# Kernel tuning notes

Hardware: AMD Instinct MI355X
Metric: run time of the kernel (lower is better)

The kernel has to match this reference:

```python
import jax, jax.numpy as jnp
import numpy as np

B, C, H, W = 2, 256, 64, 64
HEADS, DIM_HEAD = 8, 64
INNER = HEADS * DIM_HEAD


def setup_inputs() -> dict:
    key = jax.random.key(0)
    k1, k2, k3, k4 = jax.random.split(key, 4)
    x = jax.random.normal(k1, (B, C, H, W), dtype=jnp.float32)
    # 1x1 conv weights stored as [out_ch, in_ch]
    w_qkv = jax.random.normal(k2, (3 * INNER, C), dtype=jnp.float32) * (1.0 / np.sqrt(C))
    w_out = jax.random.normal(k3, (C, INNER), dtype=jnp.float32) * (1.0 / np.sqrt(INNER))
    b_out = jax.random.normal(k4, (C,), dtype=jnp.float32) * 0.01
    return {"x": x, "w_qkv": w_qkv, "w_out": w_out, "b_out": b_out}


def reference(x, w_qkv, w_out, b_out):
    b, c, h, w = x.shape
    n = h * w
    # 1x1 conv == channel matmul
    qkv = jnp.einsum('oc,bchw->bohw', w_qkv, x)  # [B, 3*inner, H, W]
    qkv = qkv.reshape(b, 3, HEADS, DIM_HEAD, n)
    qkv = jnp.transpose(qkv, (1, 0, 2, 4, 3))    # [3, B, heads, N, dim_head]
    q, k, v = qkv[0], qkv[1], qkv[2]
    scale = 1.0 / (DIM_HEAD ** 0.5)
    dots = jnp.einsum('bhnd,bhmd->bhnm', q, k) * scale  # [B, heads, N, N]
    attn = jax.nn.softmax(dots, axis=-1)
    out = jnp.einsum('bhnm,bhmd->bhnd', attn, v)        # [B, heads, N, dim_head]
    out = jnp.transpose(out, (0, 1, 3, 2)).reshape(b, INNER, h, w)
    return jnp.einsum('ci,bihw->bchw', w_out, out) + b_out[None, :, None, None]
```

## Files before the change

kernel.cpp:

```cpp
#include <hip/hip_runtime.h>
#include <hip/hip_bf16.h>

typedef unsigned short u16;
typedef __attribute__((ext_vector_type(8))) short bf16x8;
typedef __attribute__((ext_vector_type(4))) float f32x4;
typedef __attribute__((ext_vector_type(8))) unsigned short u16x8;
typedef __attribute__((ext_vector_type(4))) unsigned short u16x4;

#define N_POS 4096
#define HEADS 8
#define DHEAD 64
#define CIN   256
#define INNER 512
#define NSPLIT 2
#define JCHUNK (N_POS / NSPLIT)

__device__ __forceinline__ u16 f2bf(float f) {
    union { float f; unsigned int u; } v; v.f = f;
    unsigned int u = v.u + 0x7FFFu + ((v.u >> 16) & 1u);
    return (u16)(u >> 16);
}

__device__ __forceinline__ float bf2f(u16 h) {
    union { float f; unsigned int u; } v; v.u = ((unsigned int)h) << 16;
    return v.f;
}

__device__ __forceinline__ unsigned int pkbf2(float lo, float hi) {
    union { __hip_bfloat162 b; unsigned int u; } cv;
    cv.b = __float22bfloat162_rn(make_float2(lo, hi));
    return cv.u;
}

__global__ __launch_bounds__(256) void k0_prep(const float* __restrict__ x,
                                               const float* __restrict__ w_qkv,
                                               const float* __restrict__ w_out,
                                               u16* __restrict__ xT,
                                               u16* __restrict__ wq,
                                               u16* __restrict__ wo) {
    int bid = blockIdx.x;
    int t   = threadIdx.x;
    if (bid < 256) {
        int b = bid >> 7, rest = bid & 127;
        int n  = (rest & 15) * 256 + t;
        int c0 = (rest >> 4) * 32;
        const float* xp = x + (size_t)b * CIN * N_POS + n;
        u16* op = xT + ((size_t)(b * N_POS + n)) * CIN + c0;
        for (int g = 0; g < 4; ++g) {
            u16x8 v;
            for (int j = 0; j < 8; ++j)
                v[j] = f2bf(xp[(size_t)(c0 + g * 8 + j) * N_POS]);
            *(u16x8*)(op + g * 8) = v;
        }
    } else if (bid < 448) {
        size_t idx = (size_t)(bid - 256) * 2048 + t * 8;
        u16x8 v;
        for (int j = 0; j < 8; ++j) v[j] = f2bf(w_qkv[idx + j]);
        *(u16x8*)(wq + idx) = v;
    } else {
        size_t idx = (size_t)(bid - 448) * 2048 + t * 8;
        u16x8 v;
        for (int j = 0; j < 8; ++j) v[j] = f2bf(w_out[idx + j]);
        *(u16x8*)(wo + idx) = v;
    }
}

__global__ __launch_bounds__(256, 4) void k1_qkv(const u16* __restrict__ wq,
                                                 const u16* __restrict__ xT,
                                                 u16* __restrict__ q_ws,
                                                 u16* __restrict__ k_ws,
                                                 u16* __restrict__ vt_ws) {
    __shared__ u16 Alds[64 * 40];
    __shared__ u16 Blds[128 * 40];
    int tid = threadIdx.x;
    int n0  = blockIdx.x * 128;
    int by  = blockIdx.y;
    int b   = blockIdx.z;
    int o0  = by * 64;
    int sel = by >> 3;
    int h   = by & 7;
    int wv = tid >> 6, l = tid & 63, quad = l >> 4, l15 = l & 15;
    int srow = tid >> 2, sseg = tid & 3;
    int brow = tid >> 1, bseg = tid & 1;

    f32x4 acc[8] = {};
    for (int c0 = 0; c0 < CIN; c0 += 32) {
        *(u16x8*)&Alds[srow * 40 + sseg * 8] =
            *(const u16x8*)(wq + (size_t)(o0 + srow) * CIN + c0 + sseg * 8);
        const u16* xp = xT + ((size_t)(b * N_POS + n0 + brow)) * CIN + c0 + bseg * 16;
        *(u16x8*)&Blds[brow * 40 + bseg * 16]     = *(const u16x8*)xp;
        *(u16x8*)&Blds[brow * 40 + bseg * 16 + 8] = *(const u16x8*)(xp + 8);
        __syncthreads();
        bf16x8 af = *(const bf16x8*)&Alds[(wv * 16 + l15) * 40 + quad * 8];
        if (sel < 2) {
            for (int nt = 0; nt < 8; ++nt) {
                bf16x8 bfrag = *(const bf16x8*)&Blds[(nt * 16 + l15) * 40 + quad * 8];
                acc[nt] = __builtin_amdgcn_mfma_f32_16x16x32_bf16(af, bfrag, acc[nt], 0, 0, 0);
            }
        } else {
            for (int nt = 0; nt < 8; ++nt) {
                bf16x8 bfrag = *(const bf16x8*)&Blds[(nt * 16 + l15) * 40 + quad * 8];
                acc[nt] = __builtin_amdgcn_mfma_f32_16x16x32_bf16(bfrag, af, acc[nt], 0, 0, 0);
            }
        }
        __syncthreads();
    }
    const float QSCALE = 0.125f * 1.44269504088896f;
    int bh = b * HEADS + h;
    if (sel < 2) {
        float sc = (sel == 0) ? QSCALE : 1.0f;
        u16* base = (sel == 0) ? q_ws : k_ws;
        int dbase = wv * 16 + quad * 4;
        for (int nt = 0; nt < 8; ++nt) {
            int n = n0 + nt * 16 + l15;
            u16x4 pk;
            for (int r = 0; r < 4; ++r) pk[r] = f2bf(acc[nt][r] * sc);
            *(u16x4*)&base[((size_t)bh * N_POS + n) * DHEAD + dbase] = pk;
        }
    } else {
        int dloc = wv * 16 + l15;
        for (int nt = 0; nt < 8; ++nt) {
            u16x4 pk;
            for (int r = 0; r < 4; ++r) pk[r] = f2bf(acc[nt][r]);
            *(u16x4*)&vt_ws[((size_t)bh * DHEAD + dloc) * N_POS
                            + n0 + nt * 16 + quad * 4] = pk;
        }
    }
}

__global__ __launch_bounds__(256, 2) void k2_attn(const u16* __restrict__ q_ws,
                                                  const u16* __restrict__ k_ws,
                                                  const u16* __restrict__ vt_ws,
                                                  u16* __restrict__ op_ws,
                                                  float* __restrict__ lw_ws) {
    __shared__ u16 Klds[64 * 72];
    __shared__ u16 Vlds[64 * 72];
    int tid = threadIdx.x;
    int v   = blockIdx.x + (blockIdx.y << 4) + (blockIdx.z << 8);
    int slot = v & 7, idx = v >> 3;
    int bh   = slot * 2 + (idx & 1);
    int q0   = ((idx >> 1) & 15) * 256;
    int half = idx >> 5;
    int jbase = half * JCHUNK;
    int wv = tid >> 6, l = tid & 63, quad = l >> 4, l15 = l & 15;
    int srow = tid >> 2, sseg = tid & 3;
    int srowp = (srow & 0x23) | ((srow & 4) << 2) | ((srow & 0x18) >> 1);

    const u16* qp = q_ws + ((size_t)(bh * N_POS + q0 + wv * 64 + l15)) * DHEAD + quad * 8;
    bf16x8 bq[4][2];
    for (int it = 0; it < 4; ++it) {
        bq[it][0] = *(const bf16x8*)(qp + (size_t)it * 16 * DHEAD);
        bq[it][1] = *(const bf16x8*)(qp + (size_t)it * 16 * DHEAD + 32);
    }

    f32x4 Oacc[4][4] = {};
    float lsum[4] = {0.f, 0.f, 0.f, 0.f};

    const u16* kp = k_ws + ((size_t)(bh * N_POS + srow)) * DHEAD + sseg * 16;
    const u16* vp = vt_ws + ((size_t)(bh * DHEAD + srow)) * N_POS + sseg * 16;

    u16x8 pf0 = *(const u16x8*)(kp + (size_t)jbase * DHEAD);
    u16x8 pf1 = *(const u16x8*)(kp + (size_t)jbase * DHEAD + 8);
    u16x8 pf2 = *(const u16x8*)(vp + jbase);
    u16x8 pf3 = *(const u16x8*)(vp + jbase + 8);

    for (int j0 = jbase; j0 < jbase + JCHUNK; j0 += 64) {
        *(u16x8*)&Klds[srowp * 72 + sseg * 16]     = pf0;
        *(u16x8*)&Klds[srowp * 72 + sseg * 16 + 8] = pf1;
        *(u16x8*)&Vlds[srow * 72 + sseg * 16]      = pf2;
        *(u16x8*)&Vlds[srow * 72 + sseg * 16 + 8]  = pf3;
        __syncthreads();

        if (j0 + 64 < jbase + JCHUNK) {
            const u16* kpj = kp + (size_t)(j0 + 64) * DHEAD;
            pf0 = *(const u16x8*)kpj;
            pf1 = *(const u16x8*)(kpj + 8);
            pf2 = *(const u16x8*)(vp + j0 + 64);
            pf3 = *(const u16x8*)(vp + j0 + 72);
        }

        union PF { unsigned int u[4]; bf16x8 v; };
        PF pfr[4][2];
        for (int p = 0; p < 2; ++p)
            for (int a = 0; a < 2; ++a) {
                const u16* kb = &Klds[((2 * p + a) * 16 + l15) * 72 + quad * 8];
                bf16x8 kf0 = *(const bf16x8*)kb;
                bf16x8 kf1 = *(const bf16x8*)(kb + 32);
                f32x4 z[4];
                __builtin_amdgcn_s_setprio(1);
                for (int it = 0; it < 4; ++it) {
                    f32x4 t = {};
                    t = __builtin_amdgcn_mfma_f32_16x16x32_bf16(kf0, bq[it][0], t, 0, 0, 0);
                    t = __builtin_amdgcn_mfma_f32_16x16x32_bf16(kf1, bq[it][1], t, 0, 0, 0);
                    z[it] = t;
                }
                __builtin_amdgcn_s_setprio(0);
                for (int it = 0; it < 4; ++it) {
                    float e0 = __builtin_amdgcn_exp2f(z[it][0]);
                    float e1 = __builtin_amdgcn_exp2f(z[it][1]);
                    float e2 = __builtin_amdgcn_exp2f(z[it][2]);
                    float e3 = __builtin_amdgcn_exp2f(z[it][3]);
                    lsum[it] += (e0 + e1) + (e2 + e3);
                    pfr[it][p].u[2 * a]     = pkbf2(e0, e1);
                    pfr[it][p].u[2 * a + 1] = pkbf2(e2, e3);
                }
            }

        __builtin_amdgcn_s_setprio(1);
        for (int dt = 0; dt < 4; ++dt)
            for (int p = 0; p < 2; ++p) {
                bf16x8 vf = *(const bf16x8*)&Vlds[(dt * 16 + l15) * 72 + p * 32 + quad * 8];
                for (int it = 0; it < 4; ++it)
                    Oacc[it][dt] = __builtin_amdgcn_mfma_f32_16x16x32_bf16(vf, pfr[it][p].v, Oacc[it][dt], 0, 0, 0);
            }
        __builtin_amdgcn_s_setprio(0);
        __syncthreads();
    }

    int b = bh >> 3, h = bh & 7;
    u16* opb = op_ws + (size_t)half * 2 * N_POS * INNER;
    float* lwb = lw_ws + (size_t)half * 2 * HEADS * N_POS;
    for (int it = 0; it < 4; ++it) {
        float ls = lsum[it];
        ls += __shfl_xor(ls, 16);
        ls += __shfl_xor(ls, 32);
        int n = q0 + wv * 64 + it * 16 + l15;
        if (quad == 0) lwb[(size_t)bh * N_POS + n] = ls;
        u16* dst = opb + ((size_t)(b * N_POS + n)) * INNER + h * DHEAD;
        for (int dt = 0; dt < 4; ++dt) {
            u16x4 pk;
            for (int r = 0; r < 4; ++r) pk[r] = f2bf(Oacc[it][dt][r]);
            *(u16x4*)&dst[dt * 16 + quad * 4] = pk;
        }
    }
}

__global__ __launch_bounds__(256) void k3_out(const u16* __restrict__ wo,
                                              const float* __restrict__ b_out,
                                              const u16* __restrict__ op_ws,
                                              const float* __restrict__ lw_ws,
                                              float* __restrict__ out) {
    __shared__ u16 Alds[256 * 40];
    __shared__ u16 Blds[32 * 40];
    int tid = threadIdx.x;
    int n0 = blockIdx.x * 32;
    int b  = blockIdx.y;
    int wv = tid >> 6, l = tid & 63, quad = l >> 4, l15 = l & 15;

    f32x4 acc[4][2] = {};
    for (int i0 = 0; i0 < INNER; i0 += 32) {
        for (int rep = 0; rep < 4; ++rep) {
            int row = rep * 64 + (tid >> 2), seg = tid & 3;
            *(u16x8*)&Alds[row * 40 + seg * 8] =
                *(const u16x8*)(wo + (size_t)row * INNER + i0 + seg * 8);
        }
        if (tid < 128) {
            int srow = tid >> 2, sseg = tid & 3;
            int i = i0 + sseg * 8;
            int h = i >> 6;
            int n = n0 + srow;
            size_t lidx = ((size_t)(b * HEADS + h)) * N_POS + n;
            float ls = lw_ws[lidx] + lw_ws[(size_t)2 * HEADS * N_POS + lidx];
            float inv = 1.0f / ls;
            size_t oidx = ((size_t)(b * N_POS + n)) * INNER + i;
            u16x8 pv0 = *(const u16x8*)(op_ws + oidx);
            u16x8 pv1 = *(const u16x8*)(op_ws + (size_t)2 * N_POS * INNER + oidx);
            u16x8 vv;
            for (int k = 0; k < 8; ++k)
                vv[k] = f2bf((bf2f(pv0[k]) + bf2f(pv1[k])) * inv);
            *(u16x8*)&Blds[srow * 40 + sseg * 8] = vv;
        }
        __syncthreads();
        for (int ac = 0; ac < 4; ++ac) {
            bf16x8 af = *(const bf16x8*)&Alds[(wv * 64 + ac * 16 + l15) * 40 + quad * 8];
            for (int nt = 0; nt < 2; ++nt) {
                bf16x8 bfrag = *(const bf16x8*)&Blds[(nt * 16 + l15) * 40 + quad * 8];
                acc[ac][nt] = __builtin_amdgcn_mfma_f32_16x16x32_bf16(af, bfrag, acc[ac][nt], 0, 0, 0);
            }
        }
        __syncthreads();
    }
    for (int ac = 0; ac < 4; ++ac)
        for (int r = 0; r < 4; ++r) {
            int c = wv * 64 + ac * 16 + quad * 4 + r;
            float bias = b_out[c];
            for (int nt = 0; nt < 2; ++nt) {
                int n = n0 + nt * 16 + l15;
                out[((size_t)(b * CIN + c)) * N_POS + n] = acc[ac][nt][r] + bias;
            }
        }
}

extern "C" void kernel_launch(void* const* d_in, const int* in_sizes, int n_in,
                              void* d_out, int out_size, void* d_ws, size_t ws_size,
                              hipStream_t stream) {
    const float* x     = (const float*)d_in[0];
    const float* w_qkv = (const float*)d_in[1];
    const float* w_out = (const float*)d_in[2];
    const float* b_out = (const float*)d_in[3];
    float* out = (float*)d_out;

    u16* ws    = (u16*)d_ws;
    u16* xT    = ws;
    u16* q_ws  = xT   + (size_t)2 * N_POS * CIN;
    u16* k_ws  = q_ws + (size_t)2 * HEADS * N_POS * DHEAD;
    u16* vt_ws = k_ws + (size_t)2 * HEADS * N_POS * DHEAD;
    u16* wq_bf = vt_ws + (size_t)2 * HEADS * N_POS * DHEAD;
    u16* wo_bf = wq_bf + (size_t)3 * INNER * CIN;
    u16* op_ws = wo_bf + (size_t)CIN * INNER;
    float* lw_ws = (float*)(op_ws + (size_t)NSPLIT * 2 * N_POS * INNER);

    hipLaunchKernelGGL(k0_prep, dim3(512), dim3(256), 0, stream,
                       x, w_qkv, w_out, xT, wq_bf, wo_bf);
    hipLaunchKernelGGL(k1_qkv, dim3(32, 24, 2), dim3(256), 0, stream,
                       wq_bf, xT, q_ws, k_ws, vt_ws);
    hipLaunchKernelGGL(k2_attn, dim3(16, 16, NSPLIT), dim3(256), 0, stream,
                       q_ws, k_ws, vt_ws, op_ws, lw_ws);
    hipLaunchKernelGGL(k3_out, dim3(128, 2), dim3(256), 0, stream,
                       wo_bf, b_out, op_ws, lw_ws, out);
}
```

Measured before the change: 184.1 us.

## Double-buffer K/V LDS tiles in attention and widen output projection blocks

The attention kernel now keeps two LDS buffers for K and V. The next tile is written into the alternate buffer while the current one is consumed, which removes one __syncthreads per iteration and lets global prefetch overlap compute. Separately, the output projection kernel moves to 512 threads with 8 waves, each computing 32 output channels instead of 64, so more waves share the staging loads. The cost is doubled LDS use in attention, which may limit occupancy, and more threads per block in k3.

Measured after the change: 178.1 us. 1.03x faster.

```diff
diff --git a/kernel.cpp b/kernel.cpp
--- a/kernel.cpp
+++ b/kernel.cpp
@@ -133,8 +133,8 @@
                                                   const u16* __restrict__ vt_ws,
                                                   u16* __restrict__ op_ws,
                                                   float* __restrict__ lw_ws) {
-    __shared__ u16 Klds[64 * 72];
-    __shared__ u16 Vlds[64 * 72];
+    __shared__ u16 Klds[2][64 * 72];
+    __shared__ u16 Vlds[2][64 * 72];
     int tid = threadIdx.x;
     int v   = blockIdx.x + (blockIdx.y << 4) + (blockIdx.z << 8);
     int slot = v & 7, idx = v >> 3;
@@ -145,6 +145,8 @@
     int wv = tid >> 6, l = tid & 63, quad = l >> 4, l15 = l & 15;
     int srow = tid >> 2, sseg = tid & 3;
     int srowp = (srow & 0x23) | ((srow & 4) << 2) | ((srow & 0x18) >> 1);
+    int kofs = srowp * 72 + sseg * 16;
+    int vofs = srow * 72 + sseg * 16;
 
     const u16* qp = q_ws + ((size_t)(bh * N_POS + q0 + wv * 64 + l15)) * DHEAD + quad * 8;
     bf16x8 bq[4][2];
@@ -163,27 +165,33 @@
     u16x8 pf1 = *(const u16x8*)(kp + (size_t)jbase * DHEAD + 8);
     u16x8 pf2 = *(const u16x8*)(vp + jbase);
     u16x8 pf3 = *(const u16x8*)(vp + jbase + 8);
-
+    *(u16x8*)&Klds[0][kofs]     = pf0;
+    *(u16x8*)&Klds[0][kofs + 8] = pf1;
+    *(u16x8*)&Vlds[0][vofs]     = pf2;
+    *(u16x8*)&Vlds[0][vofs + 8] = pf3;
+    {
+        const u16* kpj = kp + (size_t)(jbase + 64) * DHEAD;
+        pf0 = *(const u16x8*)kpj;
+        pf1 = *(const u16x8*)(kpj + 8);
+        pf2 = *(const u16x8*)(vp + jbase + 64);
+        pf3 = *(const u16x8*)(vp + jbase + 72);
+    }
+    __syncthreads();
+
+    int cur = 0;
     for (int j0 = jbase; j0 < jbase + JCHUNK; j0 += 64) {
-        *(u16x8*)&Klds[srowp * 72 + sseg * 16]     = pf0;
-        *(u16x8*)&Klds[srowp * 72 + sseg * 16 + 8] = pf1;
-        *(u16x8*)&Vlds[srow * 72 + sseg * 16]      = pf2;
-        *(u16x8*)&Vlds[srow * 72 + sseg * 16 + 8]  = pf3;
-        __syncthreads();
-
         if (j0 + 64 < jbase + JCHUNK) {
-            const u16* kpj = kp + (size_t)(j0 + 64) * DHEAD;
-            pf0 = *(const u16x8*)kpj;
-            pf1 = *(const u16x8*)(kpj + 8);
-            pf2 = *(const u16x8*)(vp + j0 + 64);
-            pf3 = *(const u16x8*)(vp + j0 + 72);
+            *(u16x8*)&Klds[cur ^ 1][kofs]     = pf0;
+            *(u16x8*)&Klds[cur ^ 1][kofs + 8] = pf1;
+            *(u16x8*)&Vlds[cur ^ 1][vofs]     = pf2;
+            *(u16x8*)&Vlds[cur ^ 1][vofs + 8] = pf3;
         }
 
         union PF { unsigned int u[4]; bf16x8 v; };
         PF pfr[4][2];
         for (int p = 0; p < 2; ++p)
             for (int a = 0; a < 2; ++a) {
-                const u16* kb = &Klds[((2 * p + a) * 16 + l15) * 72 + quad * 8];
+                const u16* kb = &Klds[cur][((2 * p + a) * 16 + l15) * 72 + quad * 8];
                 bf16x8 kf0 = *(const bf16x8*)kb;
                 bf16x8 kf1 = *(const bf16x8*)(kb + 32);
                 f32x4 z[4];
@@ -209,12 +217,21 @@
         __builtin_amdgcn_s_setprio(1);
         for (int dt = 0; dt < 4; ++dt)
             for (int p = 0; p < 2; ++p) {
-                bf16x8 vf = *(const bf16x8*)&Vlds[(dt * 16 + l15) * 72 + p * 32 + quad * 8];
+                bf16x8 vf = *(const bf16x8*)&Vlds[cur][(dt * 16 + l15) * 72 + p * 32 + quad * 8];
                 for (int it = 0; it < 4; ++it)
                     Oacc[it][dt] = __builtin_amdgcn_mfma_f32_16x16x32_bf16(vf, pfr[it][p].v, Oacc[it][dt], 0, 0, 0);
             }
         __builtin_amdgcn_s_setprio(0);
-        __syncthreads();
+
+        if (j0 + 128 < jbase + JCHUNK) {
+            const u16* kpj = kp + (size_t)(j0 + 128) * DHEAD;
+            pf0 = *(const u16x8*)kpj;
+            pf1 = *(const u16x8*)(kpj + 8);
+            pf2 = *(const u16x8*)(vp + j0 + 128);
+            pf3 = *(const u16x8*)(vp + j0 + 136);
+        }
+        __syncthreads();
+        cur ^= 1;
     }
 
     int b = bh >> 3, h = bh & 7;
@@ -235,7 +252,7 @@
     }
 }
 
-__global__ __launch_bounds__(256) void k3_out(const u16* __restrict__ wo,
+__global__ __launch_bounds__(512) void k3_out(const u16* __restrict__ wo,
                                               const float* __restrict__ b_out,
                                               const u16* __restrict__ op_ws,
                                               const float* __restrict__ lw_ws,
@@ -247,12 +264,13 @@
     int b  = blockIdx.y;
     int wv = tid >> 6, l = tid & 63, quad = l >> 4, l15 = l & 15;
 
-    f32x4 acc[4][2] = {};
+    f32x4 acc[2][2] = {};
     for (int i0 = 0; i0 < INNER; i0 += 32) {
-        for (int rep = 0; rep < 4; ++rep) {
-            int row = rep * 64 + (tid >> 2), seg = tid & 3;
-            *(u16x8*)&Alds[row * 40 + seg * 8] =
-                *(const u16x8*)(wo + (size_t)row * INNER + i0 + seg * 8);
+        {
+            int row = tid >> 1, seg = tid & 1;
+            const u16* src = wo + (size_t)row * INNER + i0 + seg * 16;
+            *(u16x8*)&Alds[row * 40 + seg * 16]     = *(const u16x8*)src;
+            *(u16x8*)&Alds[row * 40 + seg * 16 + 8] = *(const u16x8*)(src + 8);
         }
         if (tid < 128) {
             int srow = tid >> 2, sseg = tid & 3;
@@ -271,8 +289,8 @@
             *(u16x8*)&Blds[srow * 40 + sseg * 8] = vv;
         }
         __syncthreads();
-        for (int ac = 0; ac < 4; ++ac) {
-            bf16x8 af = *(const bf16x8*)&Alds[(wv * 64 + ac * 16 + l15) * 40 + quad * 8];
+        for (int ac = 0; ac < 2; ++ac) {
+            bf16x8 af = *(const bf16x8*)&Alds[(wv * 32 + ac * 16 + l15) * 40 + quad * 8];
             for (int nt = 0; nt < 2; ++nt) {
                 bf16x8 bfrag = *(const bf16x8*)&Blds[(nt * 16 + l15) * 40 + quad * 8];
                 acc[ac][nt] = __builtin_amdgcn_mfma_f32_16x16x32_bf16(af, bfrag, acc[ac][nt], 0, 0, 0);
@@ -280,9 +298,9 @@
         }
         __syncthreads();
     }
-    for (int ac = 0; ac < 4; ++ac)
+    for (int ac = 0; ac < 2; ++ac)
         for (int r = 0; r < 4; ++r) {
-            int c = wv * 64 + ac * 16 + quad * 4 + r;
+            int c = wv * 32 + ac * 16 + quad * 4 + r;
             float bias = b_out[c];
             for (int nt = 0; nt < 2; ++nt) {
                 int n = n0 + nt * 16 + l15;
@@ -316,6 +334,6 @@
                        wq_bf, xT, q_ws, k_ws, vt_ws);
     hipLaunchKernelGGL(k2_attn, dim3(16, 16, NSPLIT), dim3(256), 0, stream,
                        q_ws, k_ws, vt_ws, op_ws, lw_ws);
-    hipLaunchKernelGGL(k3_out, dim3(128, 2), dim3(256), 0, stream,
+    hipLaunchKernelGGL(k3_out, dim3(128, 2), dim3(512), 0, stream,
                        wo_bf, b_out, op_ws, lw_ws, out);
 }
```
